# Optimization experiments

Hardware: AMD Instinct MI355X
Metric: run time of the kernel (lower is better)

## Reference

```python
import jax, jax.numpy as jnp
import numpy as np


def setup_inputs() -> dict:
    key = jax.random.key(0)
    ks = jax.random.split(key, 8)
    B, C, H, W = 4, 96, 128, 128
    K, N, R = 2, 1, 6  # k_group directions, d_state, dt_rank=ceil(C/16)
    f = jax.random.normal
    return {
        "x": f(ks[0], (B, C, H, W), jnp.float32),
        "in_proj_w": f(ks[1], (2 * C, C), jnp.float32) * 0.05,   # 1x1 proj -> (x, z)
        "conv_w": f(ks[2], (C, 1, 3, 3), jnp.float32) * 0.1,     # depthwise 3x3
        "conv_b": f(ks[3], (C,), jnp.float32) * 0.02,
        "x_proj_w": f(ks[4], (K, R + 2 * N, C), jnp.float32) * 0.05,
        "dt_proj_w": jax.random.uniform(ks[5], (K, C, R), jnp.float32) * 0.1,  # initialize='v2'
        "dt_proj_b": jax.random.uniform(ks[6], (K, C), jnp.float32) * 0.1,
        "A_logs": jnp.zeros((K * C, N), jnp.float32),            # initialize='v2' -> A=-1
        "Ds": jnp.ones((K * C,), jnp.float32),
        "out_norm_w": jnp.ones((C,), jnp.float32),
        "out_norm_b": jnp.zeros((C,), jnp.float32),
        "out_proj_w": f(ks[7], (C, C), jnp.float32) * 0.05,
        "scale_w": jnp.ones((1, C, 1, 1), jnp.float32),          # _ScaleModule, init 1
    }


def reference(x, in_proj_w, conv_w, conv_b, x_proj_w, dt_proj_w, dt_proj_b,
              A_logs, Ds, out_norm_w, out_norm_b, out_proj_w, scale_w):
    B, C, H, W = x.shape
    K, N = dt_proj_w.shape[0], A_logs.shape[1]
    R = dt_proj_w.shape[2]
    L = H * W

    # in_proj (Linear2d, no bias) -> split into x and gate z
    xz = jnp.einsum('oc,bchw->bohw', in_proj_w, x)
    xc, z = xz[:, :C], xz[:, C:]

    # depthwise 3x3 conv + SiLU
    xc = jax.lax.conv_general_dilated(
        xc, conv_w, (1, 1), 'SAME',
        dimension_numbers=('NCHW', 'OIHW', 'NCHW'),
        feature_group_count=C) + conv_b[None, :, None, None]
    xc = jax.nn.silu(xc)

    # bidirectional cross-scan (k_group=2): row-major flatten and its reverse
    u = xc.reshape(B, C, L)
    xs = jnp.stack([u, u[:, :, ::-1]], axis=1)                    # (B,K,C,L)

    # input-dependent dt/B/C projections
    x_dbl = jnp.einsum('bkcl,kdc->bkdl', xs, x_proj_w)            # (B,K,R+2N,L)
    dts, Bs, Cs = x_dbl[:, :, :R], x_dbl[:, :, R:R + N], x_dbl[:, :, R + N:]
    delta = jax.nn.softplus(
        jnp.einsum('bkrl,kcr->bkcl', dts, dt_proj_w) + dt_proj_b[None, :, :, None])

    A = -jnp.exp(A_logs).reshape(K, C, N)
    dA = jnp.exp(delta[..., None] * A[None, :, :, None, :])       # (B,K,C,L,N)
    dBu = (delta * xs)[..., None] * jnp.swapaxes(Bs, -1, -2)[:, :, None]  # (B,K,C,L,N)

    def step(h, inp):
        dA_l, dBu_l, C_l = inp                                    # (B,K,C,N),(B,K,C,N),(B,K,N)
        h = dA_l * h + dBu_l
        y = jnp.einsum('bkcn,bkn->bkc', h, C_l)
        return h, y

    h0 = jnp.zeros((B, K, C, N), x.dtype)
    _, ys = jax.lax.scan(step, h0, (jnp.moveaxis(dA, 3, 0),
                                    jnp.moveaxis(dBu, 3, 0),
                                    jnp.moveaxis(Cs, 3, 0)))      # ys: (L,B,K,C)
    ys = jnp.moveaxis(ys, 0, 3) + Ds.reshape(K, C)[None, :, :, None] * xs  # (B,K,C,L)

    # cross-merge: un-flip reverse direction and sum
    y = (ys[:, 0] + ys[:, 1, :, ::-1]).reshape(B, C, H, W)

    # out_norm: LayerNorm2d over channels (channel_first)
    mu = y.mean(1, keepdims=True)
    var = y.var(1, keepdims=True)
    y = (y - mu) * jax.lax.rsqrt(var + 1e-5)
    y = y * out_norm_w[None, :, None, None] + out_norm_b[None, :, None, None]

    # gate and out_proj (Linear2d, no bias)
    y = y * jax.nn.silu(z)
    out = jnp.einsum('oc,bchw->bohw', out_proj_w, y)

    # base_scale (_ScaleModule); stride=1 so no do_stride
    return scale_w * out
```

## Files before the change

### kernel.cpp

```cpp
#include <hip/hip_runtime.h>
#include <hip/hip_fp16.h>
#include <math.h>

#define Bn 4
#define Cn 96
#define Hn 128
#define Wn 128
#define Ln (Hn*Wn)
#define Kn 2
#define Rn 6
#define SC 16
#define NCH (Ln/SC)

__device__ __forceinline__ float siluf(float x) { return x / (1.f + __expf(-x)); }
__device__ __forceinline__ float softplusf(float x) {
    return fmaxf(x, 0.f) + __logf(1.f + __expf(-fabsf(x)));
}

__global__ __launch_bounds__(256, 3) void k_inproj(
    const float* __restrict__ x, const float* __restrict__ ipw,
    float* __restrict__ xc, float* __restrict__ zs)
{
    __shared__ float smem[4096 + 6272];
    float* xls = smem;
    float* wls = smem + 4096;
    float* stage = smem;

    const int t  = threadIdx.x;
    const int b  = blockIdx.x >> 7;
    const int l0 = (blockIdx.x & 127) << 7;
    const int tx = t & 15;
    const int ty = t >> 4;

    float acc[12][8];
#pragma unroll
    for (int i = 0; i < 12; ++i)
#pragma unroll
        for (int j = 0; j < 8; ++j) acc[i][j] = 0.f;

    const float* xbase = x + (size_t)b * Cn * Ln + l0;

    for (int k0 = 0; k0 < Cn; k0 += 32) {
        if (k0) __syncthreads();
        {
            int idx = t;
#pragma unroll
            for (int q = 0; q < 4; ++q, idx += 256) {
                int k = idx >> 5, p4 = idx & 31;
                *(float4*)&xls[k * 128 + p4 * 4] =
                    *(const float4*)&xbase[(size_t)(k0 + k) * Ln + p4 * 4];
            }
        }
        for (int idx = t; idx < 32 * 192; idx += 256) {
            int o = idx % 192, k = idx / 192;
            wls[k * 196 + o] = ipw[o * Cn + k0 + k];
        }
        __syncthreads();

#pragma unroll 2
        for (int kk = 0; kk < 32; ++kk) {
            float4 xv0 = *(const float4*)&xls[kk * 128 + tx * 4];
            float4 xv1 = *(const float4*)&xls[kk * 128 + 64 + tx * 4];
            const float* wrow = &wls[kk * 196 + ty * 12];
            float4 w0 = *(const float4*)&wrow[0];
            float4 w1 = *(const float4*)&wrow[4];
            float4 w2 = *(const float4*)&wrow[8];
            float wv[12] = {w0.x,w0.y,w0.z,w0.w,w1.x,w1.y,w1.z,w1.w,w2.x,w2.y,w2.z,w2.w};
            float xa[8]  = {xv0.x,xv0.y,xv0.z,xv0.w,xv1.x,xv1.y,xv1.z,xv1.w};
#pragma unroll
            for (int i = 0; i < 12; ++i)
#pragma unroll
                for (int j = 0; j < 8; ++j)
                    acc[i][j] = fmaf(wv[i], xa[j], acc[i][j]);
        }
    }

    const size_t tilebase = (size_t)b * Ln + l0;
#pragma unroll
    for (int half_ = 0; half_ < 2; ++half_) {
        __syncthreads();
        if (ty < 8) {
#pragma unroll
            for (int j = 0; j < 4; ++j)
#pragma unroll
                for (int i = 0; i < 12; ++i)
                    stage[(tx * 4 + j) * 100 + ty * 12 + i] = acc[i][half_ * 4 + j];
        }
        __syncthreads();
        {
            float4* dst = (float4*)(xc + (tilebase + half_ * 64) * Cn);
            for (int idx = t; idx < 1536; idx += 256) {
                int p = idx / 24, c4 = idx % 24;
                dst[idx] = *(const float4*)&stage[p * 100 + c4 * 4];
            }
        }
        __syncthreads();
        if (ty >= 8) {
#pragma unroll
            for (int j = 0; j < 4; ++j)
#pragma unroll
                for (int i = 0; i < 12; ++i)
                    stage[(tx * 4 + j) * 100 + (ty - 8) * 12 + i] = siluf(acc[i][half_ * 4 + j]);
        }
        __syncthreads();
        {
            float4* dst = (float4*)(zs + (tilebase + half_ * 64) * Cn);
            for (int idx = t; idx < 1536; idx += 256) {
                int p = idx / 24, c4 = idx % 24;
                dst[idx] = *(const float4*)&stage[p * 100 + c4 * 4];
            }
        }
    }
}

__global__ __launch_bounds__(256) void k_conv(
    const float* __restrict__ xc, const float* __restrict__ cw,
    const float* __restrict__ cb, float* __restrict__ u)
{
    __shared__ float cws[9 * 96];
    for (int i = threadIdx.x; i < 864; i += 256) {
        int cc = i % 96, tap = i / 96;
        cws[tap * 96 + cc] = cw[cc * 9 + tap];
    }
    __syncthreads();

    const int e   = blockIdx.x * 256 + threadIdx.x;
    const int c4  = e % 24;
    const int pos = e / 24;
    const int l   = pos % Ln;
    const int b   = pos / Ln;
    const int h   = l >> 7, w = l & 127;
    const int c   = c4 * 4;

    float4 acc = *(const float4*)&cb[c];
#pragma unroll
    for (int dh = -1; dh <= 1; ++dh) {
        int hh = h + dh;
        if (hh < 0 || hh >= Hn) continue;
#pragma unroll
        for (int dw = -1; dw <= 1; ++dw) {
            int ww = w + dw;
            if (ww < 0 || ww >= Wn) continue;
            float4 wv = *(const float4*)&cws[((dh + 1) * 3 + (dw + 1)) * 96 + c];
            float4 xv = *(const float4*)&xc[((size_t)b * Ln + (hh << 7) + ww) * Cn + c];
            acc.x = fmaf(wv.x, xv.x, acc.x);
            acc.y = fmaf(wv.y, xv.y, acc.y);
            acc.z = fmaf(wv.z, xv.z, acc.z);
            acc.w = fmaf(wv.w, xv.w, acc.w);
        }
    }
    float4 r;
    r.x = siluf(acc.x); r.y = siluf(acc.y); r.z = siluf(acc.z); r.w = siluf(acc.w);
    *(float4*)&u[((size_t)b * Ln + l) * Cn + c] = r;
}

__global__ __launch_bounds__(384, 4) void k_part1(
    const float* __restrict__ u, const float* __restrict__ xpw,
    const float* __restrict__ dtw, const float* __restrict__ dtb,
    const float* __restrict__ Alogs, const float* __restrict__ Ds,
    float* __restrict__ Pc, float* __restrict__ Qc,
    float* __restrict__ y0, __half* __restrict__ f)
{
    __shared__ float uls[32 * 100];
    __shared__ float xd[32 * 16];
    __shared__ float dsum[96];
    const int t  = threadIdx.x;
    const int j  = blockIdx.x & 511;
    const int b  = blockIdx.x >> 9;
    const int l0 = j << 5;

    {
        const float4* up4 = (const float4*)(u + ((size_t)b * Ln + l0) * Cn);
        for (int e4 = t; e4 < 768; e4 += 384) {
            int p = e4 / 24, c4 = e4 % 24;
            *(float4*)&uls[p * 100 + c4 * 4] = up4[e4];
        }
    }
    if (t < 96) dsum[t] = Ds[t] + Ds[Cn + t];
    __syncthreads();

    for (int dp = t; dp < 512; dp += 384) {
        int dd = dp & 15, p = dp >> 4;
        const float4* wr = (const float4*)(xpw + dd * Cn);
        const float4* ur = (const float4*)&uls[p * 100];
        float acc = 0.f;
#pragma unroll
        for (int c4 = 0; c4 < 24; ++c4) {
            float4 w = wr[c4], v = ur[c4];
            acc = fmaf(w.x, v.x, acc); acc = fmaf(w.y, v.y, acc);
            acc = fmaf(w.z, v.z, acc); acc = fmaf(w.w, v.w, acc);
        }
        xd[p * 16 + dd] = acc;
    }
    __syncthreads();

    const int c  = t % 96;
    const int ci = (t / 96) & 1;
    const int k  = t / 192;
    const int bk = b * Kn + k;
    const float Av = -__expf(Alogs[k * Cn + c]);
    const float bias = dtb[k * Cn + c];
    const float dsc = dsum[c];
    float dtwr[Rn];
#pragma unroll
    for (int r = 0; r < Rn; ++r) dtwr[r] = dtw[(k * Cn + c) * Rn + r];

    const int chunk = (k == 0) ? (2 * j + ci) : (1022 - 2 * j + ci);
    const int xoff = k * 8;
    __half* fkc = f + ((size_t)(b * Ln + l0) * 2 + k) * Cn + c;

    float h = 0.f, cp = 1.f;
    float yreg[SC];
#pragma unroll
    for (int hf = 0; hf < 2; ++hf) {
        float dAv[8], dBu[8], Cl[8], uv[8];
#pragma unroll
        for (int i = 0; i < 8; ++i) {
            const int ii = hf * 8 + i;
            const int p = (k == 0) ? (ci * 16 + ii) : ((1 - ci) * 16 + (15 - ii));
            const float* xr = &xd[p * 16 + xoff];
            float de = bias;
#pragma unroll
            for (int r = 0; r < Rn; ++r) de = fmaf(dtwr[r], xr[r], de);
            de = softplusf(de);
            uv[i]  = uls[p * 100 + c];
            dAv[i] = __expf(de * Av);
            dBu[i] = de * uv[i] * xr[6];
            Cl[i]  = xr[7];
        }
#pragma unroll
        for (int i = 0; i < 8; ++i) {
            const int ii = hf * 8 + i;
            const int p = (k == 0) ? (ci * 16 + ii) : ((1 - ci) * 16 + (15 - ii));
            h  = fmaf(dAv[i], h, dBu[i]);
            cp *= dAv[i];
            yreg[ii] = (k == 0) ? fmaf(dsc, uv[i], h * Cl[i]) : (h * Cl[i]);
            fkc[(size_t)p * (2 * Cn)] = __float2half(cp * Cl[i]);
        }
    }
    {
        const size_t cidx = ((size_t)bk * NCH + chunk) * Cn + c;
        Pc[cidx] = cp;
        Qc[cidx] = h;
    }

    __syncthreads();
    if (k == 0) {
#pragma unroll
        for (int i = 0; i < SC; ++i) {
            int p = ci * 16 + i;
            uls[p * 100 + c] = yreg[i];
        }
    }
    __syncthreads();
    if (k == 1) {
#pragma unroll
        for (int i = 0; i < SC; ++i) {
            int p = (1 - ci) * 16 + (15 - i);
            uls[p * 100 + c] += yreg[i];
        }
    }
    __syncthreads();
    {
        float4* y4 = (float4*)(y0 + ((size_t)b * Ln + l0) * Cn);
        for (int e4 = t; e4 < 768; e4 += 384) {
            int p = e4 / 24, c4 = e4 % 24;
            y4[e4] = *(const float4*)&uls[p * 100 + c4 * 4];
        }
    }
}

__global__ __launch_bounds__(1024) void k_scan2(
    const float* __restrict__ Pc, const float* __restrict__ Qc,
    float* __restrict__ hinit)
{
    __shared__ float Pg[32][33], Qg[32][33], gini[32][33];
    const int bk    = blockIdx.x / 3;
    const int cbase = (blockIdx.x % 3) * 32;
    const int t = threadIdx.x;
    const int c = t & 31, g = t >> 5;

    const size_t base = ((size_t)bk * NCH + g * 32) * Cn + cbase + c;
    float P = 1.f, Q = 0.f;
    for (int j = 0; j < 32; ++j) {
        size_t idx = base + (size_t)j * Cn;
        float p_ = Pc[idx], q_ = Qc[idx];
        Q = fmaf(p_, Q, q_);
        P *= p_;
    }
    Pg[g][c] = P; Qg[g][c] = Q;
    __syncthreads();
    if (t < 32) {
        float h = 0.f;
        for (int gg = 0; gg < 32; ++gg) {
            gini[gg][t] = h;
            h = fmaf(Pg[gg][t], h, Qg[gg][t]);
        }
    }
    __syncthreads();
    float h = gini[g][c];
    for (int j = 0; j < 32; ++j) {
        size_t idx = base + (size_t)j * Cn;
        hinit[idx] = h;
        h = fmaf(Pc[idx], h, Qc[idx]);
    }
}

__global__ __launch_bounds__(512) void k_merge(
    const float* __restrict__ y0, const __half* __restrict__ f,
    const float* __restrict__ hinit, const float* __restrict__ zs,
    const float* __restrict__ onw, const float* __restrict__ onb,
    const float* __restrict__ opw, const float* __restrict__ scw,
    float* __restrict__ out)
{
    __shared__ float gt[64 * 104];
    __shared__ float wls[96 * 36];
    __shared__ float h0s[4 * 96], h1s[4 * 96];
    __shared__ float mu[64], isd[64];
    const int t  = threadIdx.x;
    const int j  = blockIdx.x & 255;
    const int b  = blockIdx.x >> 8;
    const int l0 = j << 6;

    for (int idx = t; idx < 768; idx += 512) {
        if (idx < 384) {
            int q = idx / 96, c = idx % 96;
            h0s[q * 96 + c] = hinit[((size_t)(b * 2 + 0) * NCH + 4 * j + q) * Cn + c];
        } else {
            int i2 = idx - 384;
            int q = i2 / 96, c = i2 % 96;
            h1s[q * 96 + c] = hinit[((size_t)(b * 2 + 1) * NCH + (1023 - 4 * j - q)) * Cn + c];
        }
    }
    __syncthreads();

    {
        const float4* y4 = (const float4*)(y0 + ((size_t)b * Ln + l0) * Cn);
        const __half* fb = f + (size_t)(b * Ln + l0) * 2 * Cn;
        for (int e4 = t; e4 < 1536; e4 += 512) {
            int p = e4 / 24, c4 = e4 % 24;
            float4 yv = y4[e4];
            const __half* fp0 = fb + (size_t)p * (2 * Cn) + c4 * 4;
            const __half2* f0h = (const __half2*)fp0;
            const __half2* f1h = (const __half2*)(fp0 + Cn);
            float2 fa0 = __half22float2(f0h[0]);
            float2 fa1 = __half22float2(f0h[1]);
            float2 fb0 = __half22float2(f1h[0]);
            float2 fb1 = __half22float2(f1h[1]);
            const float4 h0v = *(const float4*)&h0s[(p >> 4) * 96 + c4 * 4];
            const float4 h1v = *(const float4*)&h1s[(p >> 4) * 96 + c4 * 4];
            yv.x = fmaf(h0v.x, fa0.x, fmaf(h1v.x, fb0.x, yv.x));
            yv.y = fmaf(h0v.y, fa0.y, fmaf(h1v.y, fb0.y, yv.y));
            yv.z = fmaf(h0v.z, fa1.x, fmaf(h1v.z, fb1.x, yv.z));
            yv.w = fmaf(h0v.w, fa1.y, fmaf(h1v.w, fb1.y, yv.w));
            *(float4*)&gt[p * 104 + c4 * 4] = yv;
        }
    }
    __syncthreads();

    if (t < 256) {
        const int p = t >> 2, q = t & 3;
        const float4* row = (const float4*)&gt[p * 104 + q * 24];
        float s = 0.f, ss = 0.f;
#pragma unroll
        for (int i = 0; i < 6; ++i) {
            float4 v = row[i];
            s  += v.x + v.y + v.z + v.w;
            ss += v.x*v.x + v.y*v.y + v.z*v.z + v.w*v.w;
        }
        s  += __shfl_xor(s, 1);  s  += __shfl_xor(s, 2);
        ss += __shfl_xor(ss, 1); ss += __shfl_xor(ss, 2);
        if (q == 0) {
            float m = s * (1.f / Cn);
            mu[p] = m;
            isd[p] = rsqrtf(ss * (1.f / Cn) - m * m + 1e-5f);
        }
    }
    __syncthreads();

    {
        const float4* zp4 = (const float4*)(zs + ((size_t)b * Ln + l0) * Cn);
        const float4* w4  = (const float4*)onw;
        const float4* b4  = (const float4*)onb;
        for (int e4 = t; e4 < 1536; e4 += 512) {
            int p = e4 / 24, c4 = e4 % 24;
            float4 v = *(const float4*)&gt[p * 104 + c4 * 4];
            float4 wv = w4[c4], bv = b4[c4], zv = zp4[e4];
            float m = mu[p], is = isd[p];
            v.x = ((v.x - m) * is * wv.x + bv.x) * zv.x;
            v.y = ((v.y - m) * is * wv.y + bv.y) * zv.y;
            v.z = ((v.z - m) * is * wv.z + bv.z) * zv.z;
            v.w = ((v.w - m) * is * wv.w + bv.w) * zv.w;
            *(float4*)&gt[p * 104 + c4 * 4] = v;
        }
    }

    const int og = t & 31, pg = t >> 5;
    float acc[3][4];
#pragma unroll
    for (int i = 0; i < 3; ++i)
#pragma unroll
        for (int r = 0; r < 4; ++r) acc[i][r] = 0.f;

    for (int k0 = 0; k0 < Cn; k0 += 32) {
        __syncthreads();
        for (int e4 = t; e4 < 768; e4 += 512) {
            int o = e4 >> 3, c4 = e4 & 7;
            *(float4*)&wls[o * 36 + c4 * 4] = *(const float4*)&opw[o * Cn + k0 + c4 * 4];
        }
        __syncthreads();
#pragma unroll
        for (int c4 = 0; c4 < 8; ++c4) {
            float4 w0 = *(const float4*)&wls[(og * 3 + 0) * 36 + c4 * 4];
            float4 w1 = *(const float4*)&wls[(og * 3 + 1) * 36 + c4 * 4];
            float4 w2 = *(const float4*)&wls[(og * 3 + 2) * 36 + c4 * 4];
            float4 g0 = *(const float4*)&gt[(pg * 4 + 0) * 104 + k0 + c4 * 4];
            float4 g1 = *(const float4*)&gt[(pg * 4 + 1) * 104 + k0 + c4 * 4];
            float4 g2 = *(const float4*)&gt[(pg * 4 + 2) * 104 + k0 + c4 * 4];
            float4 g3 = *(const float4*)&gt[(pg * 4 + 3) * 104 + k0 + c4 * 4];
#define ACC1(i, wv, r, gv) \
            acc[i][r] = fmaf(wv.x, gv.x, acc[i][r]); \
            acc[i][r] = fmaf(wv.y, gv.y, acc[i][r]); \
            acc[i][r] = fmaf(wv.z, gv.z, acc[i][r]); \
            acc[i][r] = fmaf(wv.w, gv.w, acc[i][r]);
            ACC1(0, w0, 0, g0) ACC1(0, w0, 1, g1) ACC1(0, w0, 2, g2) ACC1(0, w0, 3, g3)
            ACC1(1, w1, 0, g0) ACC1(1, w1, 1, g1) ACC1(1, w1, 2, g2) ACC1(1, w1, 3, g3)
            ACC1(2, w2, 0, g0) ACC1(2, w2, 1, g1) ACC1(2, w2, 2, g2) ACC1(2, w2, 3, g3)
#undef ACC1
        }
    }

    __syncthreads();
#pragma unroll
    for (int i = 0; i < 3; ++i)
#pragma unroll
        for (int r = 0; r < 4; ++r)
            gt[(og * 3 + i) * 68 + pg * 4 + r] = acc[i][r];
    __syncthreads();

    {
        float* ob = out + (size_t)b * Cn * Ln + l0;
        for (int e4 = t; e4 < 1536; e4 += 512) {
            int o = e4 >> 4, p4 = e4 & 15;
            float4 v = *(const float4*)&gt[o * 68 + p4 * 4];
            float sc = scw[o];
            v.x *= sc; v.y *= sc; v.z *= sc; v.w *= sc;
            *(float4*)&ob[(size_t)o * Ln + p4 * 4] = v;
        }
    }
}

extern "C" void kernel_launch(void* const* d_in, const int* in_sizes, int n_in,
                              void* d_out, int out_size, void* d_ws, size_t ws_size,
                              hipStream_t stream)
{
    const float* x     = (const float*)d_in[0];
    const float* ipw   = (const float*)d_in[1];
    const float* cw    = (const float*)d_in[2];
    const float* cb    = (const float*)d_in[3];
    const float* xpw   = (const float*)d_in[4];
    const float* dtw   = (const float*)d_in[5];
    const float* dtb   = (const float*)d_in[6];
    const float* Alogs = (const float*)d_in[7];
    const float* Ds    = (const float*)d_in[8];
    const float* onw   = (const float*)d_in[9];
    const float* onb   = (const float*)d_in[10];
    const float* opw   = (const float*)d_in[11];
    const float* scw   = (const float*)d_in[12];
    float* out = (float*)d_out;

    float* wsp = (float*)d_ws;
    size_t off = 0;
    float* xc   = wsp + off;
    float* y0   = wsp + off; off += (size_t)Bn * Ln * Cn;
    float* zs   = wsp + off; off += (size_t)Bn * Ln * Cn;
    float* u    = wsp + off; off += (size_t)Bn * Ln * Cn;
    __half* f   = (__half*)u;
    float* Pc    = wsp + off; off += (size_t)Bn * Kn * NCH * Cn;
    float* Qc    = wsp + off; off += (size_t)Bn * Kn * NCH * Cn;
    float* hinit = wsp + off; off += (size_t)Bn * Kn * NCH * Cn;

    k_inproj<<<Bn * 128, 256, 0, stream>>>(x, ipw, xc, zs);
    k_conv  <<<(Bn * Ln * 24) / 256, 256, 0, stream>>>(xc, cw, cb, u);
    k_part1 <<<Bn * 512, 384, 0, stream>>>(u, xpw, dtw, dtb, Alogs, Ds,
                                           Pc, Qc, y0, f);
    k_scan2 <<<24, 1024, 0, stream>>>(Pc, Qc, hinit);
    k_merge <<<Bn * 256, 512, 0, stream>>>(y0, f, hinit, zs, onw, onb,
                                           opw, scw, out);
}
```

Before: 258.1 us.

## Make k_part1 loop over four tiles with register prefetch and LDS-cached weights

Each k_part1 block now processes four consecutive 32-position tiles instead of one, so the grid shrinks by four. The x_proj weights are staged once per block in shared memory rather than read from global memory per tile. The next tile of u is prefetched into registers while the current one is computed. A separate shared buffer holds the merged y output. This amortises setup and weight loads, but it cuts the number of blocks and lowers the occupancy hint, which reduces latency hiding across the GPU.

Measured after the change: 292.2 us. 13.2% more time.

```diff
diff --git a/kernel.cpp b/kernel.cpp
--- a/kernel.cpp
+++ b/kernel.cpp
@@ -154,7 +154,7 @@
     *(float4*)&u[((size_t)b * Ln + l) * Cn + c] = r;
 }
 
-__global__ __launch_bounds__(384, 4) void k_part1(
+__global__ __launch_bounds__(384, 3) void k_part1(
     const float* __restrict__ u, const float* __restrict__ xpw,
     const float* __restrict__ dtw, const float* __restrict__ dtb,
     const float* __restrict__ Alogs, const float* __restrict__ Ds,
@@ -162,110 +162,122 @@
     float* __restrict__ y0, __half* __restrict__ f)
 {
     __shared__ float uls[32 * 100];
-    __shared__ float xd[32 * 16];
+    __shared__ float yt [32 * 100];
+    __shared__ float xd [32 * 16];
+    __shared__ float xw [16 * 100];
     __shared__ float dsum[96];
+
     const int t  = threadIdx.x;
-    const int j  = blockIdx.x & 511;
-    const int b  = blockIdx.x >> 9;
-    const int l0 = j << 5;
+    const int jb = blockIdx.x & 127;
+    const int b  = blockIdx.x >> 7;
 
     {
-        const float4* up4 = (const float4*)(u + ((size_t)b * Ln + l0) * Cn);
-        for (int e4 = t; e4 < 768; e4 += 384) {
-            int p = e4 / 24, c4 = e4 % 24;
-            *(float4*)&uls[p * 100 + c4 * 4] = up4[e4];
-        }
+        int row = t / 24, c4 = t % 24;
+        *(float4*)&xw[row * 100 + c4 * 4] = *(const float4*)&xpw[t * 4];
     }
     if (t < 96) dsum[t] = Ds[t] + Ds[Cn + t];
-    __syncthreads();
-
-    for (int dp = t; dp < 512; dp += 384) {
-        int dd = dp & 15, p = dp >> 4;
-        const float4* wr = (const float4*)(xpw + dd * Cn);
-        const float4* ur = (const float4*)&uls[p * 100];
-        float acc = 0.f;
-#pragma unroll
-        for (int c4 = 0; c4 < 24; ++c4) {
-            float4 w = wr[c4], v = ur[c4];
-            acc = fmaf(w.x, v.x, acc); acc = fmaf(w.y, v.y, acc);
-            acc = fmaf(w.z, v.z, acc); acc = fmaf(w.w, v.w, acc);
-        }
-        xd[p * 16 + dd] = acc;
-    }
-    __syncthreads();
 
     const int c  = t % 96;
     const int ci = (t / 96) & 1;
     const int k  = t / 192;
     const int bk = b * Kn + k;
-    const float Av = -__expf(Alogs[k * Cn + c]);
+    const float Av   = -__expf(Alogs[k * Cn + c]);
     const float bias = dtb[k * Cn + c];
-    const float dsc = dsum[c];
     float dtwr[Rn];
 #pragma unroll
     for (int r = 0; r < Rn; ++r) dtwr[r] = dtw[(k * Cn + c) * Rn + r];
 
-    const int chunk = (k == 0) ? (2 * j + ci) : (1022 - 2 * j + ci);
-    const int xoff = k * 8;
-    __half* fkc = f + ((size_t)(b * Ln + l0) * 2 + k) * Cn + c;
-
-    float h = 0.f, cp = 1.f;
-    float yreg[SC];
-#pragma unroll
-    for (int hf = 0; hf < 2; ++hf) {
-        float dAv[8], dBu[8], Cl[8], uv[8];
-#pragma unroll
-        for (int i = 0; i < 8; ++i) {
-            const int ii = hf * 8 + i;
-            const int p = (k == 0) ? (ci * 16 + ii) : ((1 - ci) * 16 + (15 - ii));
-            const float* xr = &xd[p * 16 + xoff];
-            float de = bias;
-#pragma unroll
-            for (int r = 0; r < Rn; ++r) de = fmaf(dtwr[r], xr[r], de);
-            de = softplusf(de);
-            uv[i]  = uls[p * 100 + c];
-            dAv[i] = __expf(de * Av);
-            dBu[i] = de * uv[i] * xr[6];
-            Cl[i]  = xr[7];
-        }
-#pragma unroll
-        for (int i = 0; i < 8; ++i) {
-            const int ii = hf * 8 + i;
-            const int p = (k == 0) ? (ci * 16 + ii) : ((1 - ci) * 16 + (15 - ii));
-            h  = fmaf(dAv[i], h, dBu[i]);
-            cp *= dAv[i];
-            yreg[ii] = (k == 0) ? fmaf(dsc, uv[i], h * Cl[i]) : (h * Cl[i]);
-            fkc[(size_t)p * (2 * Cn)] = __float2half(cp * Cl[i]);
-        }
-    }
-    {
-        const size_t cidx = ((size_t)bk * NCH + chunk) * Cn + c;
-        Pc[cidx] = cp;
-        Qc[cidx] = h;
-    }
-
-    __syncthreads();
-    if (k == 0) {
-#pragma unroll
-        for (int i = 0; i < SC; ++i) {
-            int p = ci * 16 + i;
-            uls[p * 100 + c] = yreg[i];
-        }
-    }
-    __syncthreads();
-    if (k == 1) {
-#pragma unroll
-        for (int i = 0; i < SC; ++i) {
-            int p = (1 - ci) * 16 + (15 - i);
-            uls[p * 100 + c] += yreg[i];
-        }
-    }
-    __syncthreads();
-    {
-        float4* y4 = (float4*)(y0 + ((size_t)b * Ln + l0) * Cn);
-        for (int e4 = t; e4 < 768; e4 += 384) {
-            int p = e4 / 24, c4 = e4 % 24;
-            y4[e4] = *(const float4*)&uls[p * 100 + c4 * 4];
+    const int   p0  = t / 24, c40 = t % 24;
+    const float* utile = u + ((size_t)b * Ln + (size_t)jb * 128) * Cn;
+
+    float4 nx0 = *(const float4*)&utile[t * 4];
+    float4 nx1 = *(const float4*)&utile[(t + 384) * 4];
+
+#pragma unroll 1
+    for (int tt = 0; tt < 4; ++tt) {
+        const int j  = jb * 4 + tt;
+        const int l0 = j << 5;
+
+        *(float4*)&uls[p0 * 100 + c40 * 4]        = nx0;
+        *(float4*)&uls[(p0 + 16) * 100 + c40 * 4] = nx1;
+        if (tt < 3) {
+            const float* un = utile + (size_t)(tt + 1) * 3072;
+            nx0 = *(const float4*)&un[t * 4];
+            nx1 = *(const float4*)&un[(t + 384) * 4];
+        }
+        __syncthreads();
+
+        for (int dp = t; dp < 512; dp += 384) {
+            int dd = dp & 15, p = dp >> 4;
+            const float4* wr = (const float4*)&xw[dd * 100];
+            const float4* ur = (const float4*)&uls[p * 100];
+            float acc = 0.f;
+#pragma unroll
+            for (int c4 = 0; c4 < 24; ++c4) {
+                float4 w = wr[c4], v = ur[c4];
+                acc = fmaf(w.x, v.x, acc); acc = fmaf(w.y, v.y, acc);
+                acc = fmaf(w.z, v.z, acc); acc = fmaf(w.w, v.w, acc);
+            }
+            xd[p * 16 + dd] = acc;
+        }
+        __syncthreads();
+
+        const int chunk = (k == 0) ? (2 * j + ci) : (1022 - 2 * j + ci);
+        const int xoff = k * 8;
+        __half* fkc = f + ((size_t)(b * Ln + l0) * 2 + k) * Cn + c;
+        const float dsc = dsum[c];
+
+        float h = 0.f, cp = 1.f;
+        float yreg[SC];
+#pragma unroll
+        for (int hf = 0; hf < 2; ++hf) {
+            float dAv[8], dBu[8], Cl[8], uv[8];
+#pragma unroll
+            for (int i = 0; i < 8; ++i) {
+                const int ii = hf * 8 + i;
+                const int p = (k == 0) ? (ci * 16 + ii) : ((1 - ci) * 16 + (15 - ii));
+                const float* xr = &xd[p * 16 + xoff];
+                float de = bias;
+#pragma unroll
+                for (int r = 0; r < Rn; ++r) de = fmaf(dtwr[r], xr[r], de);
+                de = softplusf(de);
+                uv[i]  = uls[p * 100 + c];
+                dAv[i] = __expf(de * Av);
+                dBu[i] = de * uv[i] * xr[6];
+                Cl[i]  = xr[7];
+            }
+#pragma unroll
+            for (int i = 0; i < 8; ++i) {
+                const int ii = hf * 8 + i;
+                const int p = (k == 0) ? (ci * 16 + ii) : ((1 - ci) * 16 + (15 - ii));
+                h  = fmaf(dAv[i], h, dBu[i]);
+                cp *= dAv[i];
+                yreg[ii] = (k == 0) ? fmaf(dsc, uv[i], h * Cl[i]) : (h * Cl[i]);
+                fkc[(size_t)p * (2 * Cn)] = __float2half(cp * Cl[i]);
+            }
+        }
+        {
+            const size_t cidx = ((size_t)bk * NCH + chunk) * Cn + c;
+            Pc[cidx] = cp;
+            Qc[cidx] = h;
+        }
+
+        if (k == 0) {
+#pragma unroll
+            for (int i = 0; i < SC; ++i)
+                yt[(ci * 16 + i) * 100 + c] = yreg[i];
+        }
+        __syncthreads();
+        if (k == 1) {
+#pragma unroll
+            for (int i = 0; i < SC; ++i)
+                yt[((1 - ci) * 16 + (15 - i)) * 100 + c] += yreg[i];
+        }
+        __syncthreads();
+        {
+            float4* y4 = (float4*)(y0 + ((size_t)b * Ln + l0) * Cn);
+            y4[t]       = *(const float4*)&yt[p0 * 100 + c40 * 4];
+            y4[t + 384] = *(const float4*)&yt[(p0 + 16) * 100 + c40 * 4];
         }
     }
 }
@@ -482,7 +494,7 @@
 
     k_inproj<<<Bn * 128, 256, 0, stream>>>(x, ipw, xc, zs);
     k_conv  <<<(Bn * Ln * 24) / 256, 256, 0, stream>>>(xc, cw, cb, u);
-    k_part1 <<<Bn * 512, 384, 0, stream>>>(u, xpw, dtw, dtb, Alogs, Ds,
+    k_part1 <<<Bn * 128, 384, 0, stream>>>(u, xpw, dtw, dtb, Alogs, Ds,
                                            Pc, Qc, y0, f);
     k_scan2 <<<24, 1024, 0, stream>>>(Pc, Qc, hinit);
     k_merge <<<Bn * 256, 512, 0, stream>>>(y0, f, hinit, zs, onw, onb,
```

## Fuse depthwise conv into scan kernel and store z and y intermediates in fp16

Applied to the files above, without the earlier changes.

Removes the standalone depthwise-conv kernel. Each scan block now loads a 3-row halo tile of xc into shared memory and computes conv+SiLU locally, so the u buffer is no longer written and read back through global memory. The gate z and partial output y0 are also stored as half precision, halving their global traffic in k_inproj, k_part1 and k_merge. This costs larger shared-memory use per block and drops the occupancy hint on k_part1, and the fp16 storage adds rounding error to z and y.

After: 266.5 us. +3.2%, slower.

```diff
diff --git a/kernel.cpp b/kernel.cpp
--- a/kernel.cpp
+++ b/kernel.cpp
@@ -17,9 +17,24 @@
     return fmaxf(x, 0.f) + __logf(1.f + __expf(-fabsf(x)));
 }
 
+__device__ __forceinline__ ushort4 pack4h(float4 v) {
+    ushort4 r;
+    r.x = __half_as_ushort(__float2half(v.x));
+    r.y = __half_as_ushort(__float2half(v.y));
+    r.z = __half_as_ushort(__float2half(v.z));
+    r.w = __half_as_ushort(__float2half(v.w));
+    return r;
+}
+__device__ __forceinline__ float4 unpack4h(const __half* p) {
+    const __half2* h2 = (const __half2*)p;
+    float2 a = __half22float2(h2[0]);
+    float2 b = __half22float2(h2[1]);
+    return make_float4(a.x, a.y, b.x, b.y);
+}
+
 __global__ __launch_bounds__(256, 3) void k_inproj(
     const float* __restrict__ x, const float* __restrict__ ipw,
-    float* __restrict__ xc, float* __restrict__ zs)
+    float* __restrict__ xc, __half* __restrict__ zs)
 {
     __shared__ float smem[4096 + 6272];
     float* xls = smem;
@@ -104,79 +119,76 @@
         }
         __syncthreads();
         {
-            float4* dst = (float4*)(zs + (tilebase + half_ * 64) * Cn);
+            __half* dst = zs + (tilebase + half_ * 64) * Cn;
             for (int idx = t; idx < 1536; idx += 256) {
                 int p = idx / 24, c4 = idx % 24;
-                dst[idx] = *(const float4*)&stage[p * 100 + c4 * 4];
+                float4 v = *(const float4*)&stage[p * 100 + c4 * 4];
+                *(ushort4*)(dst + (size_t)p * Cn + c4 * 4) = pack4h(v);
             }
         }
     }
 }
 
-__global__ __launch_bounds__(256) void k_conv(
+__global__ __launch_bounds__(384) void k_part1(
     const float* __restrict__ xc, const float* __restrict__ cw,
-    const float* __restrict__ cb, float* __restrict__ u)
-{
-    __shared__ float cws[9 * 96];
-    for (int i = threadIdx.x; i < 864; i += 256) {
-        int cc = i % 96, tap = i / 96;
-        cws[tap * 96 + cc] = cw[cc * 9 + tap];
-    }
-    __syncthreads();
-
-    const int e   = blockIdx.x * 256 + threadIdx.x;
-    const int c4  = e % 24;
-    const int pos = e / 24;
-    const int l   = pos % Ln;
-    const int b   = pos / Ln;
-    const int h   = l >> 7, w = l & 127;
-    const int c   = c4 * 4;
-
-    float4 acc = *(const float4*)&cb[c];
-#pragma unroll
-    for (int dh = -1; dh <= 1; ++dh) {
-        int hh = h + dh;
-        if (hh < 0 || hh >= Hn) continue;
-#pragma unroll
-        for (int dw = -1; dw <= 1; ++dw) {
-            int ww = w + dw;
-            if (ww < 0 || ww >= Wn) continue;
-            float4 wv = *(const float4*)&cws[((dh + 1) * 3 + (dw + 1)) * 96 + c];
-            float4 xv = *(const float4*)&xc[((size_t)b * Ln + (hh << 7) + ww) * Cn + c];
-            acc.x = fmaf(wv.x, xv.x, acc.x);
-            acc.y = fmaf(wv.y, xv.y, acc.y);
-            acc.z = fmaf(wv.z, xv.z, acc.z);
-            acc.w = fmaf(wv.w, xv.w, acc.w);
-        }
-    }
-    float4 r;
-    r.x = siluf(acc.x); r.y = siluf(acc.y); r.z = siluf(acc.z); r.w = siluf(acc.w);
-    *(float4*)&u[((size_t)b * Ln + l) * Cn + c] = r;
-}
-
-__global__ __launch_bounds__(384, 4) void k_part1(
-    const float* __restrict__ u, const float* __restrict__ xpw,
+    const float* __restrict__ cb, const float* __restrict__ xpw,
     const float* __restrict__ dtw, const float* __restrict__ dtb,
     const float* __restrict__ Alogs, const float* __restrict__ Ds,
     float* __restrict__ Pc, float* __restrict__ Qc,
-    float* __restrict__ y0, __half* __restrict__ f)
+    __half* __restrict__ y0, __half* __restrict__ f)
 {
+    __shared__ float xcl[3 * 34 * 96];
     __shared__ float uls[32 * 100];
-    __shared__ float xd[32 * 16];
+    __shared__ float xd [32 * 16];
+    __shared__ float cws[9 * 96];
     __shared__ float dsum[96];
+    float* yt = xcl + 4800;
+
     const int t  = threadIdx.x;
     const int j  = blockIdx.x & 511;
     const int b  = blockIdx.x >> 9;
+    const int h  = j >> 2;
+    const int w0 = (j & 3) << 5;
     const int l0 = j << 5;
 
     {
-        const float4* up4 = (const float4*)(u + ((size_t)b * Ln + l0) * Cn);
-        for (int e4 = t; e4 < 768; e4 += 384) {
-            int p = e4 / 24, c4 = e4 % 24;
-            *(float4*)&uls[p * 100 + c4 * 4] = up4[e4];
-        }
-    }
-    if (t < 96) dsum[t] = Ds[t] + Ds[Cn + t];
+        const float* xb = xc + (size_t)b * Ln * Cn;
+        for (int idx = t; idx < 3 * 34 * 24; idx += 384) {
+            int r = idx / (34 * 24), rem = idx % (34 * 24);
+            int wc = rem / 24, c4 = rem % 24;
+            int hh = h - 1 + r, ww = w0 - 1 + wc;
+            float4 v = make_float4(0.f, 0.f, 0.f, 0.f);
+            if (hh >= 0 && hh < Hn && ww >= 0 && ww < Wn)
+                v = *(const float4*)&xb[((size_t)(hh << 7) + ww) * Cn + c4 * 4];
+            *(float4*)&xcl[(r * 34 + wc) * 96 + c4 * 4] = v;
+        }
+        for (int i = t; i < 864; i += 384) {
+            int cc = i % 96, tap = i / 96;
+            cws[tap * 96 + cc] = cw[cc * 9 + tap];
+        }
+        if (t < 96) dsum[t] = Ds[t] + Ds[Cn + t];
+    }
+    __syncthreads();
+
+    for (int idx = t; idx < 768; idx += 384) {
+        int p = idx / 24, c4 = idx % 24;
+        float4 acc = *(const float4*)&cb[c4 * 4];
+#pragma unroll
+        for (int r = 0; r < 3; ++r)
+#pragma unroll
+            for (int dw = 0; dw < 3; ++dw) {
+                float4 wv = *(const float4*)&cws[(r * 3 + dw) * 96 + c4 * 4];
+                float4 xv = *(const float4*)&xcl[(r * 34 + p + dw) * 96 + c4 * 4];
+                acc.x = fmaf(wv.x, xv.x, acc.x);
+                acc.y = fmaf(wv.y, xv.y, acc.y);
+                acc.z = fmaf(wv.z, xv.z, acc.z);
+                acc.w = fmaf(wv.w, xv.w, acc.w);
+            }
+        float4 rr;
+        rr.x = siluf(acc.x); rr.y = siluf(acc.y);
+        rr.z = siluf(acc.z); rr.w = siluf(acc.w);
+        *(float4*)&uls[p * 100 + c4 * 4] = rr;
+    }
     __syncthreads();
 
     for (int dp = t; dp < 512; dp += 384) {
@@ -198,9 +210,9 @@
     const int ci = (t / 96) & 1;
     const int k  = t / 192;
     const int bk = b * Kn + k;
-    const float Av = -__expf(Alogs[k * Cn + c]);
+    const float Av   = -__expf(Alogs[k * Cn + c]);
     const float bias = dtb[k * Cn + c];
-    const float dsc = dsum[c];
+    const float dsc  = dsum[c];
     float dtwr[Rn];
 #pragma unroll
     for (int r = 0; r < Rn; ++r) dtwr[r] = dtw[(k * Cn + c) * Rn + r];
@@ -209,7 +221,7 @@
     const int xoff = k * 8;
     __half* fkc = f + ((size_t)(b * Ln + l0) * 2 + k) * Cn + c;
 
-    float h = 0.f, cp = 1.f;
+    float h_ = 0.f, cp = 1.f;
     float yreg[SC];
 #pragma unroll
     for (int hf = 0; hf < 2; ++hf) {
@@ -232,41 +244,37 @@
         for (int i = 0; i < 8; ++i) {
             const int ii = hf * 8 + i;
             const int p = (k == 0) ? (ci * 16 + ii) : ((1 - ci) * 16 + (15 - ii));
-            h  = fmaf(dAv[i], h, dBu[i]);
+            h_  = fmaf(dAv[i], h_, dBu[i]);
             cp *= dAv[i];
-            yreg[ii] = (k == 0) ? fmaf(dsc, uv[i], h * Cl[i]) : (h * Cl[i]);
+            yreg[ii] = (k == 0) ? fmaf(dsc, uv[i], h_ * Cl[i]) : (h_ * Cl[i]);
             fkc[(size_t)p * (2 * Cn)] = __float2half(cp * Cl[i]);
         }
     }
     {
         const size_t cidx = ((size_t)bk * NCH + chunk) * Cn + c;
         Pc[cidx] = cp;
-        Qc[cidx] = h;
-    }
-
-    __syncthreads();
+        Qc[cidx] = h_;
+    }
+
     if (k == 0) {
 #pragma unroll
-        for (int i = 0; i < SC; ++i) {
-            int p = ci * 16 + i;
-            uls[p * 100 + c] = yreg[i];
-        }
+        for (int i = 0; i < SC; ++i)
+            yt[(ci * 16 + i) * 96 + c] = yreg[i];
     }
     __syncthreads();
     if (k == 1) {
 #pragma unroll
-        for (int i = 0; i < SC; ++i) {
-            int p = (1 - ci) * 16 + (15 - i);
-            uls[p * 100 + c] += yreg[i];
-        }
-    }
-    __syncthreads();
-    {
-        float4* y4 = (float4*)(y0 + ((size_t)b * Ln + l0) * Cn);
-        for (int e4 = t; e4 < 768; e4 += 384) {
-            int p = e4 / 24, c4 = e4 % 24;
-            y4[e4] = *(const float4*)&uls[p * 100 + c4 * 4];
-        }
+        for (int i = 0; i < SC; ++i)
+            yt[((1 - ci) * 16 + (15 - i)) * 96 + c] += yreg[i];
+    }
+    __syncthreads();
+    {
+        const int p0 = t / 24, c40 = t % 24;
+        __half* yb = y0 + ((size_t)b * Ln + l0) * Cn;
+        float4 v0 = *(const float4*)&yt[p0 * 96 + c40 * 4];
+        float4 v1 = *(const float4*)&yt[(p0 + 16) * 96 + c40 * 4];
+        *(ushort4*)(yb + (size_t)p0 * Cn + c40 * 4)        = pack4h(v0);
+        *(ushort4*)(yb + (size_t)(p0 + 16) * Cn + c40 * 4) = pack4h(v1);
     }
 }
 
@@ -307,8 +315,8 @@
 }
 
 __global__ __launch_bounds__(512) void k_merge(
-    const float* __restrict__ y0, const __half* __restrict__ f,
-    const float* __restrict__ hinit, const float* __restrict__ zs,
+    const __half* __restrict__ y0, const __half* __restrict__ f,
+    const float* __restrict__ hinit, const __half* __restrict__ zs,
     const float* __restrict__ onw, const float* __restrict__ onb,
     const float* __restrict__ opw, const float* __restrict__ scw,
     float* __restrict__ out)
@@ -335,24 +343,20 @@
     __syncthreads();
 
     {
-        const float4* y4 = (const float4*)(y0 + ((size_t)b * Ln + l0) * Cn);
+        const __half* yb = y0 + ((size_t)b * Ln + l0) * Cn;
         const __half* fb = f + (size_t)(b * Ln + l0) * 2 * Cn;
         for (int e4 = t; e4 < 1536; e4 += 512) {
             int p = e4 / 24, c4 = e4 % 24;
-            float4 yv = y4[e4];
+            float4 yv = unpack4h(yb + (size_t)p * Cn + c4 * 4);
             const __half* fp0 = fb + (size_t)p * (2 * Cn) + c4 * 4;
-            const __half2* f0h = (const __half2*)fp0;
-            const __half2* f1h = (const __half2*)(fp0 + Cn);
-            float2 fa0 = __half22float2(f0h[0]);
-            float2 fa1 = __half22float2(f0h[1]);
-            float2 fb0 = __half22float2(f1h[0]);
-            float2 fb1 = __half22float2(f1h[1]);
+            float4 f0 = unpack4h(fp0);
+            float4 f1 = unpack4h(fp0 + Cn);
             const float4 h0v = *(const float4*)&h0s[(p >> 4) * 96 + c4 * 4];
             const float4 h1v = *(const float4*)&h1s[(p >> 4) * 96 + c4 * 4];
-            yv.x = fmaf(h0v.x, fa0.x, fmaf(h1v.x, fb0.x, yv.x));
-            yv.y = fmaf(h0v.y, fa0.y, fmaf(h1v.y, fb0.y, yv.y));
-            yv.z = fmaf(h0v.z, fa1.x, fmaf(h1v.z, fb1.x, yv.z));
-            yv.w = fmaf(h0v.w, fa1.y, fmaf(h1v.w, fb1.y, yv.w));
+            yv.x = fmaf(h0v.x, f0.x, fmaf(h1v.x, f1.x, yv.x));
+            yv.y = fmaf(h0v.y, f0.y, fmaf(h1v.y, f1.y, yv.y));
+            yv.z = fmaf(h0v.z, f0.z, fmaf(h1v.z, f1.z, yv.z));
+            yv.w = fmaf(h0v.w, f0.w, fmaf(h1v.w, f1.w, yv.w));
             *(float4*)&gt[p * 104 + c4 * 4] = yv;
         }
     }
@@ -379,13 +383,14 @@
     __syncthreads();
 
     {
-        const float4* zp4 = (const float4*)(zs + ((size_t)b * Ln + l0) * Cn);
+        const __half* zb = zs + ((size_t)b * Ln + l0) * Cn;
         const float4* w4  = (const float4*)onw;
         const float4* b4  = (const float4*)onb;
         for (int e4 = t; e4 < 1536; e4 += 512) {
             int p = e4 / 24, c4 = e4 % 24;
             float4 v = *(const float4*)&gt[p * 104 + c4 * 4];
-            float4 wv = w4[c4], bv = b4[c4], zv = zp4[e4];
+            float4 wv = w4[c4], bv = b4[c4];
+            float4 zv = unpack4h(zb + (size_t)p * Cn + c4 * 4);
             float m = mu[p], is = isd[p];
             v.x = ((v.x - m) * is * wv.x + bv.x) * zv.x;
             v.y = ((v.y - m) * is * wv.y + bv.y) * zv.y;
@@ -470,21 +475,20 @@
     float* out = (float*)d_out;
 
     float* wsp = (float*)d_ws;
-    size_t off = 0;
-    float* xc   = wsp + off;
-    float* y0   = wsp + off; off += (size_t)Bn * Ln * Cn;
-    float* zs   = wsp + off; off += (size_t)Bn * Ln * Cn;
-    float* u    = wsp + off; off += (size_t)Bn * Ln * Cn;
-    __half* f   = (__half*)u;
-    float* Pc    = wsp + off; off += (size_t)Bn * Kn * NCH * Cn;
-    float* Qc    = wsp + off; off += (size_t)Bn * Kn * NCH * Cn;
-    float* hinit = wsp + off; off += (size_t)Bn * Kn * NCH * Cn;
+    const size_t A = (size_t)Bn * Ln * Cn;
+    const size_t S = (size_t)Bn * Kn * NCH * Cn;
+    float*  xc   = wsp;
+    __half* zs   = (__half*)(wsp + A);
+    __half* y0h  = (__half*)(wsp + A + A / 2);
+    __half* f    = (__half*)(wsp + 2 * A);
+    float*  Pc    = wsp + 3 * A;
+    float*  Qc    = wsp + 3 * A + S;
+    float*  hinit = wsp + 3 * A + 2 * S;
 
     k_inproj<<<Bn * 128, 256, 0, stream>>>(x, ipw, xc, zs);
-    k_conv  <<<(Bn * Ln * 24) / 256, 256, 0, stream>>>(xc, cw, cb, u);
-    k_part1 <<<Bn * 512, 384, 0, stream>>>(u, xpw, dtw, dtb, Alogs, Ds,
-                                           Pc, Qc, y0, f);
+    k_part1 <<<Bn * 512, 384, 0, stream>>>(xc, cw, cb, xpw, dtw, dtb, Alogs, Ds,
+                                           Pc, Qc, y0h, f);
     k_scan2 <<<24, 1024, 0, stream>>>(Pc, Qc, hinit);
-    k_merge <<<Bn * 256, 512, 0, stream>>>(y0, f, hinit, zs, onw, onb,
+    k_merge <<<Bn * 256, 512, 0, stream>>>(y0h, f, hinit, zs, onw, onb,
                                            opw, scw, out);
 }
```
